# Kernel tuning notes

Hardware: AMD Instinct MI355X
Metric: run time of the kernel (lower is better)

## Reference

```python
import jax, jax.numpy as jnp
import numpy as np

TAU = 0.5
EPS_NORM = 1e-12  # torch F.normalize eps
EPS_DEN = 1e-8


def setup_inputs() -> dict:
    key = jax.random.key(0)
    k1, k2 = jax.random.split(key)
    N, D = 16384, 128
    z1 = jax.random.normal(k1, (N, D), dtype=jnp.float32)
    z2 = jax.random.normal(k2, (N, D), dtype=jnp.float32)
    return {"z1": z1, "z2": z2}


def _l2norm(x):
    # torch F.normalize: x / max(||x||, eps)
    n = jnp.sqrt(jnp.sum(x * x, axis=-1, keepdims=True))
    return x / jnp.maximum(n, EPS_NORM)


def reference(z1, z2):
    z1n = _l2norm(z1)
    z2n = _l2norm(z2)
    # cosine similarity of unit vectors == dot product -> single GEMM [N, N]
    sim = jnp.exp(jnp.einsum('id,jd->ij', z1n, z2n) / TAU)
    pos = jnp.exp(jnp.sum(z1n * z2n, axis=-1) / TAU)  # diagonal positives [N]
    denom = jnp.sum(sim, axis=1) + EPS_DEN
    loss = -jnp.mean(jnp.log(pos / denom))
    return loss
```

## Files before the change

### kernel.cpp

```cpp
#include <hip/hip_runtime.h>
#include <hip/hip_bf16.h>
#include <hip/hip_fp8.h>


#define N_ROWS 16384
#define DIM 128
#define JSPLIT 16
#define COLS_PER_BLOCK (N_ROWS / JSPLIT)
#define JCHUNK 32
#define NCHUNK (COLS_PER_BLOCK / JCHUNK)
#define ROWS_PER_BLOCK 128
#define ITILES (N_ROWS / ROWS_PER_BLOCK)
#define GRID_TOTAL (ITILES * JSPLIT)

#define SCALE 2.8853900817779268f

typedef __attribute__((ext_vector_type(8))) int   int8v;
typedef __attribute__((ext_vector_type(4))) int   int4v;
typedef __attribute__((ext_vector_type(4))) float floatx4;

#if __has_builtin(__builtin_amdgcn_exp2f)
#define EXP2(x) __builtin_amdgcn_exp2f(x)
#else
#define EXP2(x) exp2f(x)
#endif

__device__ inline floatx4 mfma_fp8_k128(int8v a, int8v b, floatx4 c) {
  return __builtin_amdgcn_mfma_scale_f32_16x16x128_f8f6f4(
      a, b, c, 0, 0, 0, 0x7F7F7F7F, 0, 0x7F7F7F7F);
}

__device__ inline void gload_lds16(const void* gptr, void* lptr) {
  __builtin_amdgcn_global_load_lds(
      (const __attribute__((address_space(1))) void*)gptr,
      (__attribute__((address_space(3))) void*)lptr, 16, 0, 0);
}

__device__ inline short pack_fp8x2(float x, float y) {
#if __has_builtin(__builtin_amdgcn_cvt_pk_fp8_f32)
  int p = __builtin_amdgcn_cvt_pk_fp8_f32(x, y, 0, false);
  return (short)(p & 0xFFFF);
#else
  __hip_fp8_e4m3 a(x), b(y);
  return (short)((unsigned char)a.__x | ((unsigned short)(unsigned char)b.__x << 8));
#endif
}

__global__ __launch_bounds__(256) void norm_kernel(
    const float* __restrict__ z1, const float* __restrict__ z2,
    unsigned char* __restrict__ z1q, unsigned char* __restrict__ z2q,
    float* __restrict__ diag, float* __restrict__ denom,
    float* __restrict__ out) {
  int tid = threadIdx.x;
  int wave = tid >> 6, lane = tid & 63;
  int row = blockIdx.x * 4 + wave;
  const float2* p1 = (const float2*)(z1 + (size_t)row * DIM);
  const float2* p2 = (const float2*)(z2 + (size_t)row * DIM);
  float2 a = p1[lane], b = p2[lane];
  float s11 = a.x * a.x + a.y * a.y;
  float s22 = b.x * b.x + b.y * b.y;
  float s12 = a.x * b.x + a.y * b.y;
#pragma unroll
  for (int m = 32; m >= 1; m >>= 1) {
    s11 += __shfl_xor(s11, m);
    s22 += __shfl_xor(s22, m);
    s12 += __shfl_xor(s12, m);
  }
  float inv1 = 1.0f / fmaxf(sqrtf(s11), 1e-12f);
  float inv2 = 1.0f / fmaxf(sqrtf(s22), 1e-12f);
  float sc1 = inv1 * SCALE;
  ((short*)(z1q + (size_t)row * DIM))[lane] = pack_fp8x2(a.x * sc1, a.y * sc1);
  ((short*)(z2q + (size_t)row * DIM))[lane] = pack_fp8x2(b.x * inv2, b.y * inv2);
  if (lane == 0) {
    diag[row]  = s12 * inv1 * inv2;
    denom[row] = 0.0f;
  }
  if (blockIdx.x == 0 && tid == 0) out[0] = 0.0f;
}

__global__ __launch_bounds__(256, 8) void sim_kernel(
    const unsigned char* __restrict__ z1q,
    const unsigned char* __restrict__ z2q,
    float* __restrict__ denom) {
  __shared__ int4v lds[2][JCHUNK * 8];

  int tid = threadIdx.x;
  int w   = tid >> 6;
  int q   = (tid >> 4) & 3;
  int l15 = tid & 15;
  int s   = l15 & 7;
  int itile  = blockIdx.x & (ITILES - 1);
  int jsplit = blockIdx.x >> 7;
  int i0 = itile * ROWS_PER_BLOCK + w * 32;

  const floatx4 ZERO4 = {0.f, 0.f, 0.f, 0.f};
  const floatx4 NEG4  = {-1e30f, -1e30f, -1e30f, -1e30f};

  int8v afrag[2];
#pragma unroll
  for (int ii = 0; ii < 2; ++ii) {
    const int4v* rp = (const int4v*)(z1q + (size_t)(i0 + ii * 16 + l15) * DIM);
    int8v af;
    int4v* ah = (int4v*)&af;
    ah[0] = rp[q * 2];
    ah[1] = rp[q * 2 + 1];
    afrag[ii] = af;
  }

  floatx4 rowsum[2];
  rowsum[0] = ZERO4;
  rowsum[1] = ZERO4;
  floatx4 accA = NEG4, accB = NEG4;

  const char* Bbase = (const char*)z2q + (size_t)jsplit * COLS_PER_BLOCK * DIM;

#define STAGE(cidx, bufi)                                                    \
  do {                                                                       \
    const char* _ck = Bbase + (size_t)(cidx) * JCHUNK * DIM;                 \
    char* _dst = (char*)&lds[bufi][0];                                       \
    int _row = tid >> 3, _gl = tid & 7;                                      \
    int _u = _gl ^ (_row & 7);                                               \
    int _o = 2 * (_u & 3) + (_u >> 2);                                       \
    gload_lds16(_ck + (size_t)_row * DIM + _o * 16,                          \
                _dst + (size_t)tid * 16);                                    \
  } while (0)

  STAGE(0, 0);
  __syncthreads();

  int lo_v = l15 * 8 + (q ^ s);
  int hi_v = l15 * 8 + ((q ^ s) ^ 4);

  for (int c = 0; c < NCHUNK; ++c) {
    if (c + 1 < NCHUNK) STAGE(c + 1, (c + 1) & 1);
    const int4v* buf = &lds[c & 1][0];

#pragma unroll
    for (int jj = 0; jj < 2; ++jj) {
      int8v bf;
      int4v* h = (int4v*)&bf;
      h[0] = buf[jj * 128 + lo_v];
      h[1] = buf[jj * 128 + hi_v];

      accA = mfma_fp8_k128(afrag[0], bf, ZERO4);
      {
        floatx4 e;
#pragma unroll
        for (int r = 0; r < 4; ++r) e[r] = EXP2(accB[r]);
        rowsum[1] += e;
      }
      accB = mfma_fp8_k128(afrag[1], bf, ZERO4);
      {
        floatx4 e;
#pragma unroll
        for (int r = 0; r < 4; ++r) e[r] = EXP2(accA[r]);
        rowsum[0] += e;
      }
    }
    __syncthreads();
  }
  {
    floatx4 e;
#pragma unroll
    for (int r = 0; r < 4; ++r) e[r] = EXP2(accB[r]);
    rowsum[1] += e;
  }

#pragma unroll
  for (int ii = 0; ii < 2; ++ii)
#pragma unroll
    for (int r = 0; r < 4; ++r) {
      float v = rowsum[ii][r];
      v += __shfl_xor(v, 1);
      v += __shfl_xor(v, 2);
      v += __shfl_xor(v, 4);
      v += __shfl_xor(v, 8);
      if (l15 == 0) atomicAdd(&denom[i0 + ii * 16 + q * 4 + r], v);
    }
}

__global__ __launch_bounds__(256) void loss_kernel(
    const float* __restrict__ denom, const float* __restrict__ diag,
    float* __restrict__ out) {
  int row = blockIdx.x * 256 + threadIdx.x;
  float t = 2.0f * diag[row] - __logf(denom[row] + 1e-8f);
#pragma unroll
  for (int m = 32; m >= 1; m >>= 1) t += __shfl_xor(t, m);
  if ((threadIdx.x & 63) == 0) atomicAdd(out, -t * (1.0f / N_ROWS));
}

extern "C" void kernel_launch(void* const* d_in, const int* in_sizes, int n_in,
                              void* d_out, int out_size, void* d_ws, size_t ws_size,
                              hipStream_t stream) {
  const float* z1 = (const float*)d_in[0];
  const float* z2 = (const float*)d_in[1];
  char* ws = (char*)d_ws;
  unsigned char* z1q = (unsigned char*)ws;
  unsigned char* z2q = (unsigned char*)(ws + (size_t)N_ROWS * DIM);
  float* denom = (float*)(ws + (size_t)2 * N_ROWS * DIM);
  float* diag  = (float*)(ws + (size_t)2 * N_ROWS * DIM + (size_t)N_ROWS * 4);
  float* outp  = (float*)d_out;

  norm_kernel<<<N_ROWS / 4, 256, 0, stream>>>(z1, z2, z1q, z2q, diag, denom, outp);
  sim_kernel<<<GRID_TOTAL, 256, 0, stream>>>(z1q, z2q, denom);
  loss_kernel<<<N_ROWS / 256, 256, 0, stream>>>(denom, diag, outp);
}
```

Before: 110.6 us.

## Split sim kernel into MFMA producer waves and exp consumer waves via LDS

```diff
diff --git a/kernel.cpp b/kernel.cpp
--- a/kernel.cpp
+++ b/kernel.cpp
@@ -78,46 +78,33 @@
   if (blockIdx.x == 0 && tid == 0) out[0] = 0.0f;
 }
 
-__global__ __launch_bounds__(256, 8) void sim_kernel(
+__global__ __launch_bounds__(512, 4) void sim_kernel(
     const unsigned char* __restrict__ z1q,
     const unsigned char* __restrict__ z2q,
     float* __restrict__ denom) {
-  __shared__ int4v lds[2][JCHUNK * 8];
-
-  int tid = threadIdx.x;
-  int w   = tid >> 6;
-  int q   = (tid >> 4) & 3;
-  int l15 = tid & 15;
-  int s   = l15 & 7;
+  __shared__ int4v   ldsB[2][JCHUNK * 8];
+  __shared__ floatx4 accbuf[2][4][4][64];
+
+  int tid  = threadIdx.x;
+  int wv   = tid >> 6;
+  int w    = wv & 3;
+  int prod = (wv < 4);
+  int lane = tid & 63;
+  int q    = (lane >> 4) & 3;
+  int l15  = lane & 15;
+  int s    = l15 & 7;
   int itile  = blockIdx.x & (ITILES - 1);
   int jsplit = blockIdx.x >> 7;
   int i0 = itile * ROWS_PER_BLOCK + w * 32;
 
   const floatx4 ZERO4 = {0.f, 0.f, 0.f, 0.f};
-  const floatx4 NEG4  = {-1e30f, -1e30f, -1e30f, -1e30f};
-
-  int8v afrag[2];
-#pragma unroll
-  for (int ii = 0; ii < 2; ++ii) {
-    const int4v* rp = (const int4v*)(z1q + (size_t)(i0 + ii * 16 + l15) * DIM);
-    int8v af;
-    int4v* ah = (int4v*)&af;
-    ah[0] = rp[q * 2];
-    ah[1] = rp[q * 2 + 1];
-    afrag[ii] = af;
-  }
-
-  floatx4 rowsum[2];
-  rowsum[0] = ZERO4;
-  rowsum[1] = ZERO4;
-  floatx4 accA = NEG4, accB = NEG4;
 
   const char* Bbase = (const char*)z2q + (size_t)jsplit * COLS_PER_BLOCK * DIM;
 
 #define STAGE(cidx, bufi)                                                    \
   do {                                                                       \
     const char* _ck = Bbase + (size_t)(cidx) * JCHUNK * DIM;                 \
-    char* _dst = (char*)&lds[bufi][0];                                       \
+    char* _dst = (char*)&ldsB[bufi][0];                                      \
     int _row = tid >> 3, _gl = tid & 7;                                      \
     int _u = _gl ^ (_row & 7);                                               \
     int _o = 2 * (_u & 3) + (_u >> 2);                                       \
@@ -125,58 +112,76 @@
                 _dst + (size_t)tid * 16);                                    \
   } while (0)
 
-  STAGE(0, 0);
+  int8v afrag[2];
+  if (prod) {
+#pragma unroll
+    for (int ii = 0; ii < 2; ++ii) {
+      const int4v* rp = (const int4v*)(z1q + (size_t)(i0 + ii * 16 + l15) * DIM);
+      int4v* ah = (int4v*)&afrag[ii];
+      ah[0] = rp[q * 2];
+      ah[1] = rp[q * 2 + 1];
+    }
+    STAGE(0, 0);
+  }
   __syncthreads();
 
   int lo_v = l15 * 8 + (q ^ s);
   int hi_v = l15 * 8 + ((q ^ s) ^ 4);
 
+  floatx4 rowsum[2];
+  rowsum[0] = ZERO4;
+  rowsum[1] = ZERO4;
+
   for (int c = 0; c < NCHUNK; ++c) {
-    if (c + 1 < NCHUNK) STAGE(c + 1, (c + 1) & 1);
-    const int4v* buf = &lds[c & 1][0];
-
-#pragma unroll
-    for (int jj = 0; jj < 2; ++jj) {
-      int8v bf;
-      int4v* h = (int4v*)&bf;
-      h[0] = buf[jj * 128 + lo_v];
-      h[1] = buf[jj * 128 + hi_v];
-
-      accA = mfma_fp8_k128(afrag[0], bf, ZERO4);
-      {
+    if (prod) {
+      if (c + 1 < NCHUNK) STAGE(c + 1, (c + 1) & 1);
+      const int4v* buf = &ldsB[c & 1][0];
+      floatx4 acc[4];
+#pragma unroll
+      for (int jj = 0; jj < 2; ++jj) {
+        int8v bf;
+        int4v* h = (int4v*)&bf;
+        h[0] = buf[jj * 128 + lo_v];
+        h[1] = buf[jj * 128 + hi_v];
+        acc[jj * 2 + 0] = mfma_fp8_k128(afrag[0], bf, ZERO4);
+        acc[jj * 2 + 1] = mfma_fp8_k128(afrag[1], bf, ZERO4);
+      }
+#pragma unroll
+      for (int t = 0; t < 4; ++t) accbuf[c & 1][w][t][lane] = acc[t];
+    } else if (c > 0) {
+#pragma unroll
+      for (int t = 0; t < 4; ++t) {
+        floatx4 a = accbuf[(c - 1) & 1][w][t][lane];
         floatx4 e;
 #pragma unroll
-        for (int r = 0; r < 4; ++r) e[r] = EXP2(accB[r]);
-        rowsum[1] += e;
-      }
-      accB = mfma_fp8_k128(afrag[1], bf, ZERO4);
-      {
-        floatx4 e;
-#pragma unroll
-        for (int r = 0; r < 4; ++r) e[r] = EXP2(accA[r]);
-        rowsum[0] += e;
+        for (int r = 0; r < 4; ++r) e[r] = EXP2(a[r]);
+        rowsum[t & 1] += e;
       }
     }
     __syncthreads();
   }
-  {
-    floatx4 e;
-#pragma unroll
-    for (int r = 0; r < 4; ++r) e[r] = EXP2(accB[r]);
-    rowsum[1] += e;
-  }
-
-#pragma unroll
-  for (int ii = 0; ii < 2; ++ii)
-#pragma unroll
-    for (int r = 0; r < 4; ++r) {
-      float v = rowsum[ii][r];
-      v += __shfl_xor(v, 1);
-      v += __shfl_xor(v, 2);
-      v += __shfl_xor(v, 4);
-      v += __shfl_xor(v, 8);
-      if (l15 == 0) atomicAdd(&denom[i0 + ii * 16 + q * 4 + r], v);
+
+  if (!prod) {
+#pragma unroll
+    for (int t = 0; t < 4; ++t) {
+      floatx4 a = accbuf[(NCHUNK - 1) & 1][w][t][lane];
+      floatx4 e;
+#pragma unroll
+      for (int r = 0; r < 4; ++r) e[r] = EXP2(a[r]);
+      rowsum[t & 1] += e;
     }
+#pragma unroll
+    for (int ii = 0; ii < 2; ++ii)
+#pragma unroll
+      for (int r = 0; r < 4; ++r) {
+        float v = rowsum[ii][r];
+        v += __shfl_xor(v, 1);
+        v += __shfl_xor(v, 2);
+        v += __shfl_xor(v, 4);
+        v += __shfl_xor(v, 8);
+        if (l15 == 0) atomicAdd(&denom[i0 + ii * 16 + q * 4 + r], v);
+      }
+  }
 }
 
 __global__ __launch_bounds__(256) void loss_kernel(
@@ -202,6 +207,6 @@
   float* outp  = (float*)d_out;
 
   norm_kernel<<<N_ROWS / 4, 256, 0, stream>>>(z1, z2, z1q, z2q, diag, denom, outp);
-  sim_kernel<<<GRID_TOTAL, 256, 0, stream>>>(z1q, z2q, denom);
+  sim_kernel<<<GRID_TOTAL, 512, 0, stream>>>(z1q, z2q, denom);
   loss_kernel<<<N_ROWS / 256, 256, 0, stream>>>(denom, diag, outp);
 }
```

New measurement: 128.7 us. +16.4%, slower.
